# Kernel optimization log

Measured on AMD Instinct MI355X. Metric: run time of the kernel, lower is better.

Reference implementation:

```python
import jax, jax.numpy as jnp
import numpy as np

EPS = 1e-12  # torch F.normalize eps
N, C, T = 16, 128, 16384
K, G = 64, 9  # clusters, ghost clusters


def setup_inputs() -> dict:
    key = jax.random.key(0)
    k1, k2, k3 = jax.random.split(key, 3)
    x = jax.random.normal(k1, (N, C, T), dtype=jnp.float32)
    conv_w = jax.random.normal(k2, (K + G, C), dtype=jnp.float32)  # 1x1 conv, no bias (vladv2=False)
    centroids = jax.random.uniform(k3, (K, C), dtype=jnp.float32)  # torch.rand init
    cluster_weights = jnp.ones((K,), dtype=jnp.float32)
    return {"x": x, "conv_w": conv_w, "centroids": centroids, "cluster_weights": cluster_weights}


def _l2norm(v, axis):
    return v / jnp.maximum(jnp.linalg.norm(v, axis=axis, keepdims=True), EPS)


def reference(x, conv_w, centroids, cluster_weights):
    # x: [N, C, T] (W=1 collapsed). Descriptor-wise L2 norm over channel dim.
    xn = _l2norm(x, axis=1)
    # 1x1 conv -> soft assignment logits over K+G clusters, softmax over all, keep K.
    logits = jnp.einsum('nct,kc->nkt', xn, conv_w)
    soft = jax.nn.softmax(logits, axis=1)[:, :K]  # [N, K, T]
    # VLAD: sum_t a_kt * (x_t - c_k) = (a @ x^T) - (sum_t a_kt) * c_k
    a_sum = soft.sum(axis=-1)  # [N, K]
    vlad = jnp.einsum('nkt,nct->nkc', soft, xn) - a_sum[..., None] * centroids[None]  # [N, K, C]
    # intra-normalization per cluster
    vlad = _l2norm(vlad, axis=2)
    # parametric normalization: L2-normalized cluster weights
    cw = cluster_weights / jnp.maximum(jnp.linalg.norm(cluster_weights), EPS)
    vlad = vlad * cw[None, :, None]
    v = vlad.reshape(vlad.shape[0], -1)  # [N, K*C]
    return _l2norm(v, axis=1)
```

## Files before the change

kernel.cpp:

```cpp
#include <hip/hip_runtime.h>
#include <math.h>

#define N_  16
#define C_  128
#define T_  16384
#define K_  64
#define KG_ 73
#define CT  512
#define NCH 32
#define EPSN 1e-12f
#define P1  72
#define P2  72

typedef __bf16 bf16x4v __attribute__((ext_vector_type(4)));
typedef __bf16 bf16x8v __attribute__((ext_vector_type(8)));
typedef float  f32x4v  __attribute__((ext_vector_type(4)));

#define MFMA(a, b, c) __builtin_amdgcn_mfma_f32_16x16x32_bf16((a), (b), (c), 0, 0, 0)

__global__ __launch_bounds__(256, 2)
void k_main(const float* __restrict__ x, const float* __restrict__ conv_w,
            float* __restrict__ gaccp, float* __restrict__ gasump)
{
    __shared__ __align__(16) __bf16 xb[2][C_ * P1];
    __shared__ __align__(16) __bf16 st[2][K_ * P2];
    __shared__ float asq[4 * K_];

    const int tid  = threadIdx.x;
    const int lane = tid & 63;
    const int wv   = __builtin_amdgcn_readfirstlane(tid >> 6);
    const int q    = lane >> 4;
    const int l15  = lane & 15;
    const int n     = blockIdx.x >> 5;
    const int chunk = blockIdx.x & 31;
    const int t0    = chunk * CT;

    bf16x8v wf[5][4];
#pragma unroll
    for (int nt = 0; nt < 5; ++nt) {
        const int row = min(16 * nt + l15, KG_ - 1);
#pragma unroll
        for (int ks = 0; ks < 4; ++ks) {
            const float* wp = conv_w + (size_t)row * C_ + 32 * ks + 8 * q;
            const float4 w0 = *(const float4*)wp;
            const float4 w1 = *(const float4*)(wp + 4);
            bf16x8v f;
            f[0] = (__bf16)w0.x; f[1] = (__bf16)w0.y; f[2] = (__bf16)w0.z; f[3] = (__bf16)w0.w;
            f[4] = (__bf16)w1.x; f[5] = (__bf16)w1.y; f[6] = (__bf16)w1.z; f[7] = (__bf16)w1.w;
            wf[nt][ks] = f;
        }
    }

    f32x4v acc2[8];
#pragma unroll
    for (int i = 0; i < 8; ++i) acc2[i] = (f32x4v){0.f, 0.f, 0.f, 0.f};
    float asum_acc[4] = {0.f, 0.f, 0.f, 0.f};

    const int cst = tid >> 4, t4 = tid & 15;
    const float* xbase = x + ((size_t)(n * C_ + cst)) * T_ + 4 * t4;

    const float* g1 = x + ((size_t)(n * C_ + 8 * q)) * T_ + t0 + 16 * wv + l15;

    float4 pf[8];
#pragma unroll
    for (int r = 0; r < 8; ++r)
        pf[r] = *(const float4*)(xbase + (size_t)r * 16 * T_ + t0);

    int p = 0;
    for (int it = 0; it < 8; ++it) {
#pragma unroll
        for (int r = 0; r < 8; ++r) {
            bf16x4v v = { (__bf16)pf[r].x, (__bf16)pf[r].y, (__bf16)pf[r].z, (__bf16)pf[r].w };
            *(bf16x4v*)&xb[p][(cst + 16 * r) * P1 + 4 * t4] = v;
        }

        if (it < 7) {
            const int tb = t0 + (it + 1) * 64;
#pragma unroll
            for (int r = 0; r < 8; ++r)
                pf[r] = *(const float4*)(xbase + (size_t)r * 16 * T_ + tb);
        }

        f32x4v acc1[5];
#pragma unroll
        for (int i = 0; i < 5; ++i) acc1[i] = (f32x4v){0.f, 0.f, 0.f, 0.f};
        f32x4v gr = (f32x4v){0.f, 0.f, 0.f, 0.f};

#pragma unroll
        for (int ks = 0; ks < 4; ++ks) {
            const float* gp = g1 + ((size_t)(32 * ks)) * T_ + it * 64;
            bf16x8v af;
#pragma unroll
            for (int j = 0; j < 8; ++j) af[j] = (__bf16)gp[(size_t)j * T_];
            gr = MFMA(af, af, gr);
#pragma unroll
            for (int nt = 0; nt < 5; ++nt)
                acc1[nt] = MFMA(af, wf[nt][ks], acc1[nt]);
        }

        float rn[4];
#pragma unroll
        for (int r = 0; r < 4; ++r) {
            const float ss = __int_as_float(
                __builtin_amdgcn_ds_bpermute((20 * q + r) << 2, __float_as_int(gr[r])));
            rn[r] = 1.f / fmaxf(sqrtf(ss), EPSN);
        }

        float e[5][4];
        float d[4] = {0.f, 0.f, 0.f, 0.f};
#pragma unroll
        for (int nt = 0; nt < 5; ++nt) {
            const bool valid = (16 * nt + l15) < KG_;
#pragma unroll
            for (int r = 0; r < 4; ++r) {
                const float ev = __expf(acc1[nt][r] * rn[r]);
                e[nt][r] = valid ? ev : 0.f;
                d[r] += e[nt][r];
            }
        }
#pragma unroll
        for (int r = 0; r < 4; ++r) {
            d[r] += __shfl_xor(d[r], 1);
            d[r] += __shfl_xor(d[r], 2);
            d[r] += __shfl_xor(d[r], 4);
            d[r] += __shfl_xor(d[r], 8);
            d[r] = 1.f / d[r];
        }

#pragma unroll
        for (int nt = 0; nt < 4; ++nt) {
            bf16x4v sv;
            float ap = 0.f;
#pragma unroll
            for (int r = 0; r < 4; ++r) {
                const float s = e[nt][r] * d[r];
                ap += s;
                sv[r] = (__bf16)(s * rn[r]);
            }
            asum_acc[nt] += ap;
            *(bf16x4v*)&st[p][(16 * nt + l15) * P2 + 16 * wv + 4 * q] = sv;
        }
        __syncthreads();

        {
            const int clp = wv >> 1;
            const int chh = wv & 1;
            bf16x8v sa[2][2];
#pragma unroll
            for (int clb = 0; clb < 2; ++clb)
#pragma unroll
                for (int ks2 = 0; ks2 < 2; ++ks2)
                    sa[clb][ks2] = *(const bf16x8v*)
                        &st[p][(16 * (2 * clp + clb) + l15) * P2 + 32 * ks2 + 8 * q];
#pragma unroll
            for (int cb = 0; cb < 4; ++cb) {
                const int c = 16 * (4 * chh + cb) + l15;
                const bf16x8v xf0 = *(const bf16x8v*)&xb[p][c * P1 + 8 * q];
                const bf16x8v xf1 = *(const bf16x8v*)&xb[p][c * P1 + 32 + 8 * q];
                acc2[cb]     = MFMA(sa[0][0], xf0, acc2[cb]);
                acc2[cb]     = MFMA(sa[0][1], xf1, acc2[cb]);
                acc2[4 + cb] = MFMA(sa[1][0], xf0, acc2[4 + cb]);
                acc2[4 + cb] = MFMA(sa[1][1], xf1, acc2[4 + cb]);
            }
        }
        p ^= 1;
    }

    {
        const int clp = wv >> 1, chh = wv & 1;
        float* gp = gaccp + ((size_t)(n * NCH + chunk) * K_) * C_;
#pragma unroll
        for (int clb = 0; clb < 2; ++clb)
#pragma unroll
            for (int cb = 0; cb < 4; ++cb)
#pragma unroll
                for (int r = 0; r < 4; ++r) {
                    const int cl = 16 * (2 * clp + clb) + 4 * q + r;
                    const int c  = 16 * (4 * chh + cb) + l15;
                    gp[cl * C_ + c] = acc2[clb * 4 + cb][r];
                }
    }

#pragma unroll
    for (int nt = 0; nt < 4; ++nt) {
        float v = asum_acc[nt];
        v += __shfl_xor(v, 16);
        v += __shfl_xor(v, 32);
        if (q == 0) asq[wv * K_ + 16 * nt + l15] = v;
    }
    __syncthreads();
    if (tid < K_) {
        const float s = asq[tid] + asq[K_ + tid] + asq[2 * K_ + tid] + asq[3 * K_ + tid];
        gasump[(n * NCH + chunk) * K_ + tid] = s;
    }
}

__global__ __launch_bounds__(64)
void k_post(const float* __restrict__ gaccp, const float* __restrict__ gasump,
            const float* __restrict__ centroids, const float* __restrict__ cwv,
            float* __restrict__ out, float* __restrict__ nsq)
{
    const int b = blockIdx.x;
    const int n = b >> 6, k = b & 63;
    const int lane = threadIdx.x;

    const float cv = cwv[lane];
    float cs = cv * cv;
#pragma unroll
    for (int off = 32; off; off >>= 1) cs += __shfl_xor(cs, off);
    const float cwn = cwv[k] / fmaxf(sqrtf(cs), EPSN);

    float v0 = 0.f, v1 = 0.f;
    const float* gp = gaccp + ((size_t)(n * NCH) * K_ + k) * C_;
    for (int ch = 0; ch < NCH; ++ch) {
        v0 += gp[lane];
        v1 += gp[lane + 64];
        gp += K_ * C_;
    }
    float asum = 0.f;
    const float* gs = gasump + (size_t)(n * NCH) * K_ + k;
    for (int ch = 0; ch < NCH; ++ch) asum += gs[ch * K_];

    const float* ce = centroids + (size_t)k * C_;
    v0 -= asum * ce[lane];
    v1 -= asum * ce[lane + 64];
    float ss = v0 * v0 + v1 * v1;
#pragma unroll
    for (int off = 32; off; off >>= 1) ss += __shfl_xor(ss, off);
    const float scale = cwn / fmaxf(sqrtf(ss), EPSN);

    float* o = out + (size_t)n * (K_ * C_) + (size_t)k * C_;
    o[lane]      = v0 * scale;
    o[lane + 64] = v1 * scale;
    if (lane == 0) atomicAdd(&nsq[n], ss * scale * scale);
}

__global__ __launch_bounds__(256)
void k_norm(float* __restrict__ out, const float* __restrict__ nsq)
{
    const int i = blockIdx.x * 256 + threadIdx.x;
    const int n = i >> 13;
    const float r = 1.f / fmaxf(sqrtf(nsq[n]), EPSN);
    out[i] *= r;
}

extern "C" void kernel_launch(void* const* d_in, const int* in_sizes, int n_in,
                              void* d_out, int out_size, void* d_ws, size_t ws_size,
                              hipStream_t stream)
{
    const float* x         = (const float*)d_in[0];
    const float* conv_w    = (const float*)d_in[1];
    const float* centroids = (const float*)d_in[2];
    const float* cweights  = (const float*)d_in[3];
    float* out = (float*)d_out;

    float* nsq    = (float*)d_ws;
    float* gasump = nsq + 16;
    float* gaccp  = gasump + N_ * NCH * K_;

    hipMemsetAsync(nsq, 0, N_ * sizeof(float), stream);
    hipLaunchKernelGGL(k_main, dim3(N_ * NCH), dim3(256), 0, stream,
                       x, conv_w, gaccp, gasump);
    hipLaunchKernelGGL(k_post, dim3(N_ * K_), dim3(64), 0, stream,
                       gaccp, gasump, centroids, cweights, out, nsq);
    hipLaunchKernelGGL(k_norm, dim3(N_ * K_ * C_ / 256), dim3(256), 0, stream,
                       out, nsq);
}
```

Baseline: 228.1 us.

## Load x once per thread for both MFMA fragments and LDS staging, swizzle LDS

```diff
diff --git a/kernel.cpp b/kernel.cpp
--- a/kernel.cpp
+++ b/kernel.cpp
@@ -56,46 +56,50 @@
     for (int i = 0; i < 8; ++i) acc2[i] = (f32x4v){0.f, 0.f, 0.f, 0.f};
     float asum_acc[4] = {0.f, 0.f, 0.f, 0.f};
 
-    const int cst = tid >> 4, t4 = tid & 15;
-    const float* xbase = x + ((size_t)(n * C_ + cst)) * T_ + 4 * t4;
-
     const float* g1 = x + ((size_t)(n * C_ + 8 * q)) * T_ + t0 + 16 * wv + l15;
 
-    float4 pf[8];
-#pragma unroll
-    for (int r = 0; r < 8; ++r)
-        pf[r] = *(const float4*)(xbase + (size_t)r * 16 * T_ + t0);
+    float pfA[32];
+#pragma unroll
+    for (int ks = 0; ks < 4; ++ks)
+#pragma unroll
+        for (int j = 0; j < 8; ++j)
+            pfA[8 * ks + j] = g1[(size_t)(32 * ks + j) * T_];
+
+    const int tpos = 8 * ((2 * wv + (l15 >> 3)) ^ q) + (l15 & 7);
 
     int p = 0;
     for (int it = 0; it < 8; ++it) {
-#pragma unroll
-        for (int r = 0; r < 8; ++r) {
-            bf16x4v v = { (__bf16)pf[r].x, (__bf16)pf[r].y, (__bf16)pf[r].z, (__bf16)pf[r].w };
-            *(bf16x4v*)&xb[p][(cst + 16 * r) * P1 + 4 * t4] = v;
-        }
+        bf16x8v af[4];
+#pragma unroll
+        for (int ks = 0; ks < 4; ++ks)
+#pragma unroll
+            for (int j = 0; j < 8; ++j)
+                af[ks][j] = (__bf16)pfA[8 * ks + j];
+
+#pragma unroll
+        for (int ks = 0; ks < 4; ++ks)
+#pragma unroll
+            for (int j = 0; j < 8; ++j)
+                xb[p][(32 * ks + 8 * q + j) * P1 + tpos] = af[ks][j];
 
         if (it < 7) {
-            const int tb = t0 + (it + 1) * 64;
-#pragma unroll
-            for (int r = 0; r < 8; ++r)
-                pf[r] = *(const float4*)(xbase + (size_t)r * 16 * T_ + tb);
+#pragma unroll
+            for (int ks = 0; ks < 4; ++ks)
+#pragma unroll
+                for (int j = 0; j < 8; ++j)
+                    pfA[8 * ks + j] = g1[(size_t)(32 * ks + j) * T_ + (it + 1) * 64];
         }
 
         f32x4v acc1[5];
 #pragma unroll
         for (int i = 0; i < 5; ++i) acc1[i] = (f32x4v){0.f, 0.f, 0.f, 0.f};
         f32x4v gr = (f32x4v){0.f, 0.f, 0.f, 0.f};
-
 #pragma unroll
         for (int ks = 0; ks < 4; ++ks) {
-            const float* gp = g1 + ((size_t)(32 * ks)) * T_ + it * 64;
-            bf16x8v af;
-#pragma unroll
-            for (int j = 0; j < 8; ++j) af[j] = (__bf16)gp[(size_t)j * T_];
-            gr = MFMA(af, af, gr);
+            gr = MFMA(af[ks], af[ks], gr);
 #pragma unroll
             for (int nt = 0; nt < 5; ++nt)
-                acc1[nt] = MFMA(af, wf[nt][ks], acc1[nt]);
+                acc1[nt] = MFMA(af[ks], wf[nt][ks], acc1[nt]);
         }
 
         float rn[4];
@@ -154,9 +158,12 @@
                         &st[p][(16 * (2 * clp + clb) + l15) * P2 + 32 * ks2 + 8 * q];
 #pragma unroll
             for (int cb = 0; cb < 4; ++cb) {
-                const int c = 16 * (4 * chh + cb) + l15;
-                const bf16x8v xf0 = *(const bf16x8v*)&xb[p][c * P1 + 8 * q];
-                const bf16x8v xf1 = *(const bf16x8v*)&xb[p][c * P1 + 32 + 8 * q];
+                const int nt2 = 4 * chh + cb;
+                const int c = 16 * nt2 + l15;
+                const int g = (2 * nt2 + (l15 >> 3)) & 3;
+                const int koff = 8 * (q ^ g);
+                const bf16x8v xf0 = *(const bf16x8v*)&xb[p][c * P1 + koff];
+                const bf16x8v xf1 = *(const bf16x8v*)&xb[p][c * P1 + koff + 32];
                 acc2[cb]     = MFMA(sa[0][0], xf0, acc2[cb]);
                 acc2[cb]     = MFMA(sa[0][1], xf1, acc2[cb]);
                 acc2[4 + cb] = MFMA(sa[1][0], xf0, acc2[4 + cb]);
@@ -195,44 +202,59 @@
     }
 }
 
-__global__ __launch_bounds__(64)
+__global__ __launch_bounds__(256)
 void k_post(const float* __restrict__ gaccp, const float* __restrict__ gasump,
             const float* __restrict__ centroids, const float* __restrict__ cwv,
             float* __restrict__ out, float* __restrict__ nsq)
 {
+    __shared__ float red[4 * C_];
+    __shared__ float ras[4];
     const int b = blockIdx.x;
     const int n = b >> 6, k = b & 63;
-    const int lane = threadIdx.x;
-
-    const float cv = cwv[lane];
-    float cs = cv * cv;
-#pragma unroll
-    for (int off = 32; off; off >>= 1) cs += __shfl_xor(cs, off);
-    const float cwn = cwv[k] / fmaxf(sqrtf(cs), EPSN);
-
+    const int tid = threadIdx.x, w = tid >> 6, lane = tid & 63;
+
+    const float* gp = gaccp + ((size_t)(n * NCH) * K_ + k) * C_;
     float v0 = 0.f, v1 = 0.f;
-    const float* gp = gaccp + ((size_t)(n * NCH) * K_ + k) * C_;
-    for (int ch = 0; ch < NCH; ++ch) {
-        v0 += gp[lane];
-        v1 += gp[lane + 64];
-        gp += K_ * C_;
-    }
-    float asum = 0.f;
+#pragma unroll
+    for (int j = 0; j < 8; ++j) {
+        const size_t off = (size_t)(8 * w + j) * K_ * C_;
+        v0 += gp[off + lane];
+        v1 += gp[off + lane + 64];
+    }
+    float as = 0.f;
     const float* gs = gasump + (size_t)(n * NCH) * K_ + k;
-    for (int ch = 0; ch < NCH; ++ch) asum += gs[ch * K_];
-
-    const float* ce = centroids + (size_t)k * C_;
-    v0 -= asum * ce[lane];
-    v1 -= asum * ce[lane + 64];
-    float ss = v0 * v0 + v1 * v1;
-#pragma unroll
-    for (int off = 32; off; off >>= 1) ss += __shfl_xor(ss, off);
-    const float scale = cwn / fmaxf(sqrtf(ss), EPSN);
-
-    float* o = out + (size_t)n * (K_ * C_) + (size_t)k * C_;
-    o[lane]      = v0 * scale;
-    o[lane + 64] = v1 * scale;
-    if (lane == 0) atomicAdd(&nsq[n], ss * scale * scale);
+#pragma unroll
+    for (int j = 0; j < 8; ++j) as += gs[(8 * w + j) * K_];
+
+    red[w * C_ + lane]      = v0;
+    red[w * C_ + 64 + lane] = v1;
+    if (lane == 0) ras[w] = as;
+    __syncthreads();
+
+    if (w == 0) {
+        v0 = red[lane] + red[C_ + lane] + red[2 * C_ + lane] + red[3 * C_ + lane];
+        v1 = red[64 + lane] + red[C_ + 64 + lane] + red[2 * C_ + 64 + lane] + red[3 * C_ + 64 + lane];
+        const float asum = ras[0] + ras[1] + ras[2] + ras[3];
+
+        const float cv = cwv[lane];
+        float cs = cv * cv;
+#pragma unroll
+        for (int off = 32; off; off >>= 1) cs += __shfl_xor(cs, off);
+        const float cwn = cwv[k] / fmaxf(sqrtf(cs), EPSN);
+
+        const float* ce = centroids + (size_t)k * C_;
+        v0 -= asum * ce[lane];
+        v1 -= asum * ce[lane + 64];
+        float ss = v0 * v0 + v1 * v1;
+#pragma unroll
+        for (int off = 32; off; off >>= 1) ss += __shfl_xor(ss, off);
+        const float scale = cwn / fmaxf(sqrtf(ss), EPSN);
+
+        float* o = out + (size_t)n * (K_ * C_) + (size_t)k * C_;
+        o[lane]      = v0 * scale;
+        o[lane + 64] = v1 * scale;
+        if (lane == 0) atomicAdd(&nsq[n], ss * scale * scale);
+    }
 }
 
 __global__ __launch_bounds__(256)
@@ -261,7 +283,7 @@
     hipMemsetAsync(nsq, 0, N_ * sizeof(float), stream);
     hipLaunchKernelGGL(k_main, dim3(N_ * NCH), dim3(256), 0, stream,
                        x, conv_w, gaccp, gasump);
-    hipLaunchKernelGGL(k_post, dim3(N_ * K_), dim3(64), 0, stream,
+    hipLaunchKernelGGL(k_post, dim3(N_ * K_), dim3(256), 0, stream,
                        gaccp, gasump, centroids, cweights, out, nsq);
     hipLaunchKernelGGL(k_norm, dim3(N_ * K_ * C_ / 256), dim3(256), 0, stream,
                        out, nsq);
```

Result: no change. 229.2 us (+0.5%).
